# Performance work log

Measured on AMD Instinct MI355X. Metric: run time of the kernel, lower is better.

Reference implementation:

```python
import jax, jax.numpy as jnp
import numpy as np

TOP_K = 2
BALANCE_W = 0.01


def setup_inputs() -> dict:
    key = jax.random.key(0)
    ks = jax.random.split(key, 9)
    B, T, D, E, H, S = 4, 2048, 1024, 16, 1024, 2

    def w(k, shape):
        return jax.random.normal(k, shape, jnp.float32) * 0.02

    return {
        "x": jax.random.normal(ks[0], (B, T, D), jnp.float32),
        "router_w": w(ks[1], (D, E)),
        "router_bias": jnp.zeros((E,), jnp.float32),
        "Wg": w(ks[2], (E, D, H)),
        "Wu": w(ks[3], (E, D, H)),
        "Wd": w(ks[4], (E, H, D)),
        "sWg": w(ks[5], (D, S * H)),
        "sWu": w(ks[6], (D, S * H)),
        "sWd": w(ks[7], (S * H, D)),
    }


def reference(x, router_w, router_bias, Wg, Wu, Wd, sWg, sWu, sWd):
    B, T, D = x.shape
    E = router_w.shape[1]
    flat = x.reshape(-1, D)                      # [N, D], N = B*T
    N = flat.shape[0]

    # ---- router (fp32, matching x.float() in torch ref) ----
    logits = flat @ router_w                     # [N, E]
    probs = jax.nn.softmax(logits, axis=-1)      # unbiased probs
    _, indices = jax.lax.top_k(logits + router_bias, TOP_K)  # [N, K]
    weights = jnp.take_along_axis(probs, indices, axis=-1)   # [N, K]
    weights = weights / jnp.maximum(weights.sum(-1, keepdims=True), 1e-9)

    # per-(token, expert) combine weight; top-k indices are unique per row
    C = jnp.zeros((N, E), flat.dtype).at[jnp.arange(N)[:, None], indices].add(weights)
    expert_load = jax.nn.one_hot(indices, E, dtype=jnp.float32).sum((0, 1))  # [E]

    # ---- routed SwiGLU experts: scan over experts, masked combine ----
    def body(acc, per_e):
        wg, wu, wd, c = per_e                    # [D,H],[D,H],[H,D],[N]
        h = jax.nn.silu(flat @ wg) * (flat @ wu) # [N, H]
        return acc + (h @ wd) * c[:, None], None

    routed, _ = jax.lax.scan(body, jnp.zeros_like(flat), (Wg, Wu, Wd, C.T))

    # ---- shared expert ----
    shared = (jax.nn.silu(flat @ sWg) * (flat @ sWu)) @ sWd

    out = (routed + shared).reshape(B, T, D)

    # ---- Switch/DeepSeek balance loss (training mode) ----
    expert_fraction = expert_load / (N * TOP_K)
    probability_fraction = probs.mean(0)
    balance = BALANCE_W * E * jnp.sum(expert_fraction * probability_fraction)

    return out, balance, expert_load
```

## Files before the change

kernel.cpp:

```cpp
#include <hip/hip_runtime.h>
#include <stdint.h>

#define N_TOK 8192
#define DDIM  1024
#define NEXP  16
#define HDIM  1024
#define SHDIM 2048
#define TM 128
#define BK 64
#define MT_R 144

#define SH_GU_NT  (SHDIM / 64)
#define SH_GU_WGS ((N_TOK / TM) * SH_GU_NT)
#define RT_GU_NT  (HDIM / 64)
#define RT_GU_WGS (MT_R * RT_GU_NT)
#define GU_WGS    (SH_GU_WGS + RT_GU_WGS)

#define TND 128
#define DN_NT     (DDIM / TND)
#define SH_DN_WGS ((N_TOK / TM) * DN_NT)
#define RT_DN_WGS (MT_R * DN_NT)
#define DN_WGS    (SH_DN_WGS + RT_DN_WGS)

#define CPAD 16

typedef __bf16 bf16x8 __attribute__((ext_vector_type(8)));
typedef float  f32x4  __attribute__((ext_vector_type(4)));

__device__ __forceinline__ unsigned short f2bf(float f) {
  union { float f; unsigned u; } v; v.f = f;
  unsigned r = v.u + 0x7fffu + ((v.u >> 16) & 1u);
  return (unsigned short)(r >> 16);
}
__device__ __forceinline__ float bf2f(unsigned short u) {
  union { unsigned u; float f; } v; v.u = (unsigned)u << 16; return v.f;
}

__device__ __forceinline__ void gload16(const void* g, void* l) {
  __builtin_amdgcn_global_load_lds(
      (const __attribute__((address_space(1))) void*)g,
      (__attribute__((address_space(3))) void*)l, 16, 0, 0);
}

__device__ __forceinline__ int xcd_swizzle() {
  int nwg = (int)gridDim.x;
  int b = (int)blockIdx.x;
  return (b & 7) * (nwg >> 3) + (b >> 3);
}


__global__ void k_zero(int* cnt, int* cursor, float* probsum) {
  int t = threadIdx.x;
  if (t < NEXP * CPAD) { cnt[t] = 0; cursor[t] = 0; probsum[t] = 0.f; }
}

__global__ __launch_bounds__(256) void k_router(
    const float* __restrict__ x, const float* __restrict__ rw,
    const float* __restrict__ rb, int* __restrict__ cnt,
    int* __restrict__ tok_idx, float* __restrict__ tok_w,
    float* __restrict__ probs, unsigned short* __restrict__ Xbf) {
  __shared__ float rwT[NEXP * 1024];
  const int t = threadIdx.x;
  {
    int dbase = t >> 2, e0 = (t & 3) * 4;
#pragma unroll
    for (int c = 0; c < 16; c++) {
      int d = dbase + 64 * c;
      float4 v = *(const float4*)(rw + (size_t)d * NEXP + e0);
      rwT[(e0 + 0) * 1024 + d] = v.x;
      rwT[(e0 + 1) * 1024 + d] = v.y;
      rwT[(e0 + 2) * 1024 + d] = v.z;
      rwT[(e0 + 3) * 1024 + d] = v.w;
    }
  }
  __syncthreads();
  const int lane = t & 63, wv = t >> 6;
  const int tok0 = blockIdx.x * 16 + wv * 4;
  float acc[4][NEXP];
#pragma unroll
  for (int tt = 0; tt < 4; tt++)
#pragma unroll
    for (int e = 0; e < NEXP; e++) acc[tt][e] = 0.f;

#pragma unroll
  for (int c = 0; c < 4; c++) {
    int d = lane * 4 + 256 * c;
    float4 xv[4];
#pragma unroll
    for (int tt = 0; tt < 4; tt++) {
      xv[tt] = *(const float4*)(x + (size_t)(tok0 + tt) * DDIM + d);
      ushort4 o;
      o.x = f2bf(xv[tt].x); o.y = f2bf(xv[tt].y);
      o.z = f2bf(xv[tt].z); o.w = f2bf(xv[tt].w);
      *(ushort4*)(Xbf + (size_t)(tok0 + tt) * DDIM + d) = o;
    }
#pragma unroll
    for (int e = 0; e < NEXP; e++) {
      float4 w4 = *(const float4*)(&rwT[e * 1024 + d]);
#pragma unroll
      for (int tt = 0; tt < 4; tt++) {
        acc[tt][e] = fmaf(xv[tt].x, w4.x, acc[tt][e]);
        acc[tt][e] = fmaf(xv[tt].y, w4.y, acc[tt][e]);
        acc[tt][e] = fmaf(xv[tt].z, w4.z, acc[tt][e]);
        acc[tt][e] = fmaf(xv[tt].w, w4.w, acc[tt][e]);
      }
    }
  }
#pragma unroll
  for (int tt = 0; tt < 4; tt++)
#pragma unroll
    for (int e = 0; e < NEXP; e++) {
      float v = acc[tt][e];
#pragma unroll
      for (int o = 32; o; o >>= 1) v += __shfl_xor(v, o);
      acc[tt][e] = v;
    }

#pragma unroll
  for (int tt = 0; tt < 4; tt++) {
    if (lane == tt) {
      int tok = tok0 + tt;
      float mx = acc[tt][0];
#pragma unroll
      for (int e = 1; e < NEXP; e++) mx = fmaxf(mx, acc[tt][e]);
      float p[NEXP]; float s = 0.f;
#pragma unroll
      for (int e = 0; e < NEXP; e++) { p[e] = __expf(acc[tt][e] - mx); s += p[e]; }
      float inv = 1.f / s;
      float* pdst = probs + (size_t)tok * NEXP;
#pragma unroll
      for (int e = 0; e < NEXP; e++) { p[e] *= inv; pdst[e] = p[e]; }
      int i0 = 0; float b0 = acc[tt][0] + rb[0];
#pragma unroll
      for (int e = 1; e < NEXP; e++) { float v = acc[tt][e] + rb[e]; if (v > b0) { b0 = v; i0 = e; } }
      int i1 = -1; float b1 = -3.4e38f;
#pragma unroll
      for (int e = 0; e < NEXP; e++) {
        if (e == i0) continue;
        float v = acc[tt][e] + rb[e]; if (v > b1) { b1 = v; i1 = e; }
      }
      float w0 = 0.f, w1 = 0.f;
#pragma unroll
      for (int e = 0; e < NEXP; e++) { if (e == i0) w0 = p[e]; if (e == i1) w1 = p[e]; }
      float ssum = fmaxf(w0 + w1, 1e-9f);
      w0 /= ssum; w1 /= ssum;
      atomicAdd(&cnt[i0 * CPAD], 1); atomicAdd(&cnt[i1 * CPAD], 1);
      tok_idx[tok * 2]     = i0; tok_idx[tok * 2 + 1] = i1;
      tok_w[tok * 2]       = w0; tok_w[tok * 2 + 1]   = w1;
    }
  }
}

__global__ __launch_bounds__(256) void k_psum(
    const float* __restrict__ probs, float* __restrict__ probsum) {
  __shared__ float ps[NEXP];
  const int t = threadIdx.x;
  if (t < NEXP) ps[t] = 0.f;
  __syncthreads();
  int e = t & 15, trow = t >> 4;
  float s = 0.f;
#pragma unroll
  for (int c = 0; c < 8; c++) {
    int tok = blockIdx.x * 128 + c * 16 + trow;
    s += probs[(size_t)tok * NEXP + e];
  }
  atomicAdd(&ps[e], s);
  __syncthreads();
  if (t < NEXP) atomicAdd(&probsum[t * CPAD], ps[t]);
}

__global__ void k_prefix(const int* __restrict__ cnt, int* __restrict__ offs) {
  if (threadIdx.x == 0) {
    int o = 0;
    for (int e = 0; e < NEXP; e++) { offs[e] = o; o += ((cnt[e * CPAD] + 127) & ~127); }
    offs[NEXP] = o;
  }
}

__global__ __launch_bounds__(256) void k_assign(
    const int* __restrict__ tok_idx, const float* __restrict__ tok_w,
    int* __restrict__ cursor, const int* __restrict__ offs,
    int* __restrict__ row_token, int* __restrict__ tok_rows) {
  int i = blockIdx.x * 256 + threadIdx.x;
  if (i >= N_TOK * 2) return;
  int e = tok_idx[i];
  int pos = atomicAdd(&cursor[e * CPAD], 1);
  int row = offs[e] + pos;
  row_token[row] = i >> 1;
  tok_rows[i] = row;
}


__device__ __forceinline__ void do_transpose64(
    const float* __restrict__ src, unsigned short* __restrict__ dst,
    int R, int C, int tc, int tr, float* tile ) {
  int rx = threadIdx.x >> 4;
  int cx = (threadIdx.x & 15) * 4;
#pragma unroll
  for (int p = 0; p < 4; p++) {
    int r = p * 16 + rx;
    float4 v = *(const float4*)(src + (size_t)(tr + r) * C + tc + cx);
    tile[(cx + 0) * 65 + r] = v.x;
    tile[(cx + 1) * 65 + r] = v.y;
    tile[(cx + 2) * 65 + r] = v.z;
    tile[(cx + 3) * 65 + r] = v.w;
  }
  __syncthreads();
#pragma unroll
  for (int p = 0; p < 4; p++) {
    int c = p * 16 + rx;
    float v0 = tile[c * 65 + cx + 0];
    float v1 = tile[c * 65 + cx + 1];
    float v2 = tile[c * 65 + cx + 2];
    float v3 = tile[c * 65 + cx + 3];
    ushort4 o; o.x = f2bf(v0); o.y = f2bf(v1); o.z = f2bf(v2); o.w = f2bf(v3);
    *(ushort4*)(dst + (size_t)(tc + c) * R + tr + cx) = o;
  }
}

__global__ __launch_bounds__(256) void k_transpose_big(
    const float* __restrict__ Wg, const float* __restrict__ Wu,
    const float* __restrict__ Wd, unsigned short* __restrict__ WgT,
    unsigned short* __restrict__ WuT, unsigned short* __restrict__ WdT) {
  __shared__ float tile[64 * 65];
  int id = blockIdx.x;
  int which = id >> 12;
  int rem = id & 4095;
  int mat = rem >> 8;
  int tl  = rem & 255;
  int bx = tl & 15, by = tl >> 4;
  const float* src = (which == 0 ? Wg : which == 1 ? Wu : Wd) + (size_t)mat * 1024 * 1024;
  unsigned short* dst = (which == 0 ? WgT : which == 1 ? WuT : WdT) + (size_t)mat * 1024 * 1024;
  do_transpose64(src, dst, 1024, 1024, bx * 64, by * 64, tile);
}

__global__ __launch_bounds__(256) void k_transpose_sh(
    const float* __restrict__ sWg, const float* __restrict__ sWu,
    const float* __restrict__ sWd, unsigned short* __restrict__ sWgT,
    unsigned short* __restrict__ sWuT, unsigned short* __restrict__ sWdT) {
  __shared__ float tile[64 * 65];
  int id = blockIdx.x;
  if (id < 1024) {
    const float* src = id < 512 ? sWg : sWu;
    unsigned short* dst = id < 512 ? sWgT : sWuT;
    int tl = id & 511;
    int bx = tl & 31, by = tl >> 5;
    do_transpose64(src, dst, 1024, 2048, bx * 64, by * 64, tile);
  } else {
    int tl = id - 1024;
    int bx = tl & 15, by = tl >> 4;
    do_transpose64(sWd, sWdT, 2048, 1024, bx * 64, by * 64, tile);
  }
}


__global__ __launch_bounds__(256, 4) void k_gateup_all(
    const unsigned short* __restrict__ Xbf,
    const unsigned short* __restrict__ sWgT,
    const unsigned short* __restrict__ sWuT,
    const unsigned short* __restrict__ WgT,
    const unsigned short* __restrict__ WuT,
    unsigned short* __restrict__ Hs,
    unsigned short* __restrict__ Hr,
    const int* __restrict__ offs, const int* __restrict__ cnt,
    const int* __restrict__ row_token) {
  __shared__ unsigned short As[TM * BK];
  __shared__ unsigned short Bgs[64 * BK];
  __shared__ unsigned short Bus[64 * BK];

  const int wg = xcd_swizzle();
  const int t = threadIdx.x;
  const int lane = t & 63, wv = t >> 6;
  const int lr  = lane >> 3;
  const int kbx = (lane & 7) ^ lr;

  int tm, tn, validEnd, Nh;
  const unsigned short *Bgp, *Bup;
  unsigned short* Hout;
  const unsigned short* pA[4];

  if (wg < SH_GU_WGS) {
    int band = wg >> 9;
    int r = wg & 511;
    tm = (r >> 3) * TM;
    tn = (band * 8 + (r & 7)) * 64;
    validEnd = 0x7fffffff;
    Bgp = sWgT; Bup = sWuT;
    Hout = Hs; Nh = SHDIM;
#pragma unroll
    for (int j = 0; j < 4; j++)
      pA[j] = Xbf + (size_t)(tm + (wv * 4 + j) * 8 + lr) * DDIM;
  } else {
    int u = wg - SH_GU_WGS;
    int band = u / 1152;
    int r = u % 1152;
    tm = (r >> 3) * TM;
    tn = (band * 8 + (r & 7)) * 64;
    if (tm >= offs[NEXP]) return;
    int e = 0;
#pragma unroll
    for (int i = 1; i < NEXP; i++) if (tm >= offs[i]) e = i;
    validEnd = offs[e] + cnt[e * CPAD];
    Bgp = WgT + (size_t)e * HDIM * DDIM;
    Bup = WuT + (size_t)e * HDIM * DDIM;
    Hout = Hr; Nh = HDIM;
#pragma unroll
    for (int j = 0; j < 4; j++) {
      int row = tm + (wv * 4 + j) * 8 + lr;
      int tok = row < validEnd ? row_token[row] : 0;
      pA[j] = Xbf + (size_t)tok * DDIM;
    }
  }
  const unsigned short* pBg[2];
  const unsigned short* pBu[2];
#pragma unroll
  for (int j = 0; j < 2; j++) {
    int row = tn + (wv * 2 + j) * 8 + lr;
    pBg[j] = Bgp + (size_t)row * DDIM;
    pBu[j] = Bup + (size_t)row * DDIM;
  }

  auto stage = [&](int k0) {
#pragma unroll
    for (int j = 0; j < 4; j++)
      gload16(pA[j] + k0 + kbx * 8, (void*)&As[(wv * 4 + j) * 512]);
#pragma unroll
    for (int j = 0; j < 2; j++) {
      gload16(pBg[j] + k0 + kbx * 8, (void*)&Bgs[(wv * 2 + j) * 512]);
      gload16(pBu[j] + k0 + kbx * 8, (void*)&Bus[(wv * 2 + j) * 512]);
    }
  };

  f32x4 accG[4][2] = {};
  f32x4 accU[4][2] = {};
  const int wr = wv >> 1, wc = wv & 1;
  const int rbase = lane & 15;
  const int kgrp = lane >> 4;

  for (int k0 = 0; k0 < DDIM; k0 += BK) {
    if (k0) __syncthreads();
    stage(k0);
    __syncthreads();
#pragma unroll
    for (int kk = 0; kk < 2; kk++) {
      bf16x8 af[4], gf[2], uf[2];
      int kbl = kk * 4 + kgrp;
#pragma unroll
      for (int i = 0; i < 4; i++) {
        int r = wr * 64 + i * 16 + rbase;
        af[i] = *(const bf16x8*)((const char*)&As[0] + r * 128 + ((kbl ^ (r & 7)) << 4));
      }
#pragma unroll
      for (int j = 0; j < 2; j++) {
        int r = wc * 32 + j * 16 + rbase;
        gf[j] = *(const bf16x8*)((const char*)&Bgs[0] + r * 128 + ((kbl ^ (r & 7)) << 4));
        uf[j] = *(const bf16x8*)((const char*)&Bus[0] + r * 128 + ((kbl ^ (r & 7)) << 4));
      }
#pragma unroll
      for (int i = 0; i < 4; i++)
#pragma unroll
        for (int j = 0; j < 2; j++) {
          accG[i][j] = __builtin_amdgcn_mfma_f32_16x16x32_bf16(af[i], gf[j], accG[i][j], 0, 0, 0);
          accU[i][j] = __builtin_amdgcn_mfma_f32_16x16x32_bf16(af[i], uf[j], accU[i][j], 0, 0, 0);
        }
    }
  }

  const int orow0 = tm + wr * 64 + (lane >> 4) * 4;
  const int ocol0 = tn + wc * 32 + (lane & 15);
#pragma unroll
  for (int i = 0; i < 4; i++)
#pragma unroll
    for (int j = 0; j < 2; j++)
#pragma unroll
      for (int r = 0; r < 4; r++) {
        int row = orow0 + i * 16 + r;
        if (row < validEnd) {
          float g = accG[i][j][r], u = accU[i][j][r];
          float h = g / (1.f + __expf(-g)) * u;
          Hout[(size_t)row * Nh + ocol0 + j * 16] = f2bf(h);
        }
      }
}

__global__ __launch_bounds__(256, 4) void k_down_all(
    const unsigned short* __restrict__ Hs,
    const unsigned short* __restrict__ Hr,
    const unsigned short* __restrict__ sWdT,
    const unsigned short* __restrict__ WdT,
    float* __restrict__ out,
    unsigned short* __restrict__ Rbuf,
    const int* __restrict__ offs, const int* __restrict__ cnt) {
  __shared__ unsigned short As[TM * BK];
  __shared__ unsigned short Bs[TND * BK];

  const int wg = xcd_swizzle();
  const int t = threadIdx.x;
  const int lane = t & 63, wv = t >> 6;
  const int lr  = lane >> 3;
  const int kbx = (lane & 7) ^ lr;

  int tm, tn, validEnd, K;
  bool routed;
  const unsigned short* pA[4];
  const unsigned short* pB[4];

  if (wg < SH_DN_WGS) {
    routed = false; K = SHDIM;
    tm = (wg >> 3) * TM;
    tn = (wg & 7) * TND;
    validEnd = 0x7fffffff;
#pragma unroll
    for (int j = 0; j < 4; j++) {
      pA[j] = Hs + (size_t)(tm + (wv * 4 + j) * 8 + lr) * SHDIM;
      pB[j] = sWdT + (size_t)(tn + (wv * 4 + j) * 8 + lr) * SHDIM;
    }
  } else {
    routed = true; K = HDIM;
    int wgr = wg - SH_DN_WGS;
    tm = (wgr >> 3) * TM;
    tn = (wgr & 7) * TND;
    if (tm >= offs[NEXP]) return;
    int e = 0;
#pragma unroll
    for (int i = 1; i < NEXP; i++) if (tm >= offs[i]) e = i;
    validEnd = offs[e] + cnt[e * CPAD];
    const unsigned short* B = WdT + (size_t)e * DDIM * HDIM;
#pragma unroll
    for (int j = 0; j < 4; j++) {
      pA[j] = Hr + (size_t)(tm + (wv * 4 + j) * 8 + lr) * HDIM;
      pB[j] = B + (size_t)(tn + (wv * 4 + j) * 8 + lr) * HDIM;
    }
  }

  auto stage = [&](int k0) {
#pragma unroll
    for (int j = 0; j < 4; j++) {
      gload16(pA[j] + k0 + kbx * 8, (void*)&As[(wv * 4 + j) * 512]);
      gload16(pB[j] + k0 + kbx * 8, (void*)&Bs[(wv * 4 + j) * 512]);
    }
  };

  f32x4 acc[4][4] = {};
  const int wr = wv >> 1, wc = wv & 1;
  const int rbase = lane & 15;
  const int kgrp = lane >> 4;

  for (int k0 = 0; k0 < K; k0 += BK) {
    if (k0) __syncthreads();
    stage(k0);
    __syncthreads();
#pragma unroll
    for (int kk = 0; kk < 2; kk++) {
      bf16x8 af[4], bf[4];
      int kbl = kk * 4 + kgrp;
#pragma unroll
      for (int i = 0; i < 4; i++) {
        int r = wr * 64 + i * 16 + rbase;
        af[i] = *(const bf16x8*)((const char*)&As[0] + r * 128 + ((kbl ^ (r & 7)) << 4));
      }
#pragma unroll
      for (int j = 0; j < 4; j++) {
        int r = wc * 64 + j * 16 + rbase;
        bf[j] = *(const bf16x8*)((const char*)&Bs[0] + r * 128 + ((kbl ^ (r & 7)) << 4));
      }
#pragma unroll
      for (int i = 0; i < 4; i++)
#pragma unroll
        for (int j = 0; j < 4; j++)
          acc[i][j] = __builtin_amdgcn_mfma_f32_16x16x32_bf16(af[i], bf[j], acc[i][j], 0, 0, 0);
    }
  }

  const int orow0 = tm + wr * 64 + (lane >> 4) * 4;
  const int ocol0 = tn + wc * 64 + (lane & 15);
#pragma unroll
  for (int i = 0; i < 4; i++)
#pragma unroll
    for (int j = 0; j < 4; j++)
#pragma unroll
      for (int r = 0; r < 4; r++) {
        int row = orow0 + i * 16 + r;
        int col = ocol0 + j * 16;
        if (routed) {
          if (row < validEnd) Rbuf[(size_t)row * DDIM + col] = f2bf(acc[i][j][r]);
        } else {
          out[(size_t)row * DDIM + col] = acc[i][j][r];
        }
      }
}

__global__ __launch_bounds__(256) void k_combine(
    float* __restrict__ out, const unsigned short* __restrict__ Rbuf,
    const int* __restrict__ tok_rows, const float* __restrict__ tok_w) {
  int tok = blockIdx.x;
  int c = threadIdx.x;
  int r0 = tok_rows[tok * 2], r1 = tok_rows[tok * 2 + 1];
  float w0 = tok_w[tok * 2],  w1 = tok_w[tok * 2 + 1];
  float4 o  = ((const float4*)(out + (size_t)tok * DDIM))[c];
  ushort4 a = ((const ushort4*)(Rbuf + (size_t)r0 * DDIM))[c];
  ushort4 b = ((const ushort4*)(Rbuf + (size_t)r1 * DDIM))[c];
  o.x += w0 * bf2f(a.x) + w1 * bf2f(b.x);
  o.y += w0 * bf2f(a.y) + w1 * bf2f(b.y);
  o.z += w0 * bf2f(a.z) + w1 * bf2f(b.z);
  o.w += w0 * bf2f(a.w) + w1 * bf2f(b.w);
  ((float4*)(out + (size_t)tok * DDIM))[c] = o;
}

__global__ void k_tail(const float* __restrict__ probsum, const int* __restrict__ cnt,
                       float* __restrict__ out_tail) {
  if (threadIdx.x == 0) {
    float bal = 0.f;
    for (int e = 0; e < NEXP; e++) {
      float frac = (float)cnt[e * CPAD] / (float)(N_TOK * 2);
      bal += frac * (probsum[e * CPAD] / (float)N_TOK);
    }
    out_tail[0] = 0.01f * (float)NEXP * bal;
  }
  if (threadIdx.x < NEXP) out_tail[1 + threadIdx.x] = (float)cnt[threadIdx.x * CPAD];
}


extern "C" void kernel_launch(void* const* d_in, const int* in_sizes, int n_in,
                              void* d_out, int out_size, void* d_ws, size_t ws_size,
                              hipStream_t stream) {
  const float* x   = (const float*)d_in[0];
  const float* rw  = (const float*)d_in[1];
  const float* rb  = (const float*)d_in[2];
  const float* Wg  = (const float*)d_in[3];
  const float* Wu  = (const float*)d_in[4];
  const float* Wd  = (const float*)d_in[5];
  const float* sWg = (const float*)d_in[6];
  const float* sWu = (const float*)d_in[7];
  const float* sWd = (const float*)d_in[8];
  float* out = (float*)d_out;

  uint8_t* w = (uint8_t*)d_ws;
  size_t off = 0;
  auto alloc = [&](size_t bytes) -> void* {
    void* p = w + off;
    off += (bytes + 255) & ~(size_t)255;
    return p;
  };

  int*   cnt      = (int*)alloc(NEXP * CPAD * 4);
  int*   cursor   = (int*)alloc(NEXP * CPAD * 4);
  float* probsum  = (float*)alloc(NEXP * CPAD * 4);
  int*   offs     = (int*)alloc((NEXP + 1) * 4);
  int*   tok_idx  = (int*)alloc((size_t)N_TOK * 2 * 4);
  float* tok_w    = (float*)alloc((size_t)N_TOK * 2 * 4);
  int*   tok_rows = (int*)alloc((size_t)N_TOK * 2 * 4);
  int*   row_tok  = (int*)alloc((size_t)MT_R * TM * 4);
  float* probs    = (float*)alloc((size_t)N_TOK * NEXP * 4);
  unsigned short* Xbf  = (unsigned short*)alloc((size_t)N_TOK * DDIM * 2);
  unsigned short* Hs   = (unsigned short*)alloc((size_t)N_TOK * SHDIM * 2);
  unsigned short* Hr   = (unsigned short*)alloc((size_t)MT_R * TM * HDIM * 2);
  unsigned short* Rbuf = (unsigned short*)alloc((size_t)MT_R * TM * DDIM * 2);
  unsigned short* WgT  = (unsigned short*)alloc((size_t)NEXP * HDIM * DDIM * 2);
  unsigned short* WuT  = (unsigned short*)alloc((size_t)NEXP * HDIM * DDIM * 2);
  unsigned short* WdT  = (unsigned short*)alloc((size_t)NEXP * DDIM * HDIM * 2);
  unsigned short* sWgT = (unsigned short*)alloc((size_t)SHDIM * DDIM * 2);
  unsigned short* sWuT = (unsigned short*)alloc((size_t)SHDIM * DDIM * 2);
  unsigned short* sWdT = (unsigned short*)alloc((size_t)DDIM * SHDIM * 2);

  if (off > ws_size) return;

  k_zero<<<1, 256, 0, stream>>>(cnt, cursor, probsum);
  k_router<<<N_TOK / 16, 256, 0, stream>>>(x, rw, rb, cnt, tok_idx, tok_w, probs, Xbf);
  k_psum<<<64, 256, 0, stream>>>(probs, probsum);
  k_prefix<<<1, 1, 0, stream>>>(cnt, offs);
  k_assign<<<(N_TOK * 2) / 256, 256, 0, stream>>>(tok_idx, tok_w, cursor, offs, row_tok, tok_rows);

  k_transpose_big<<<12288, 256, 0, stream>>>(Wg, Wu, Wd, WgT, WuT, WdT);
  k_transpose_sh<<<1536, 256, 0, stream>>>(sWg, sWu, sWd, sWgT, sWuT, sWdT);

  k_gateup_all<<<GU_WGS, 256, 0, stream>>>(
      Xbf, sWgT, sWuT, WgT, WuT, Hs, Hr, offs, cnt, row_tok);
  k_down_all<<<DN_WGS, 256, 0, stream>>>(
      Hs, Hr, sWdT, WdT, out, Rbuf, offs, cnt);
  k_combine<<<N_TOK, 256, 0, stream>>>(out, Rbuf, tok_rows, tok_w);

  k_tail<<<1, 32, 0, stream>>>(probsum, cnt, out + (size_t)N_TOK * DDIM);
}
```

Before: 426.5 us.

## Fuse router bookkeeping kernels and overlap down-weight transposes with gate-up GEMM

Folds the probability-sum reduction into the router via shared-memory atomics, which removes the probs buffer and the k_psum launch. Prefix offsets are now recomputed per block from the counts, which removes k_prefix. The assign step is merged into the gate/up weight transpose kernel, and the down-projection weight transposes run as extra workgroups inside the gate-up GEMM launch so they overlap with its compute. The balance-loss tail moves into the combine kernel and the occupancy hint is raised to 5. In exchange it adds per-block redundant offset computation and couples transpose work with GEMM scheduling.

```diff
diff --git a/kernel.cpp b/kernel.cpp
--- a/kernel.cpp
+++ b/kernel.cpp
@@ -10,17 +10,22 @@
 #define BK 64
 #define MT_R 144
 
-#define SH_GU_NT  (SHDIM / 64)
-#define SH_GU_WGS ((N_TOK / TM) * SH_GU_NT)
-#define RT_GU_NT  (HDIM / 64)
-#define RT_GU_WGS (MT_R * RT_GU_NT)
-#define GU_WGS    (SH_GU_WGS + RT_GU_WGS)
+#define SH_GU_NT  32
+#define SH_GU_WGS 2048
+#define RT_GU_NT  16
+#define RT_GU_WGS 2304
+#define GU_WGS    4352
+#define GU_SLOTS  (GU_WGS / 8)
+#define TR2_WGS   4608
+#define TR2_SLOTS (TR2_WGS / 8)
+#define GUF_WGS   (GU_WGS + TR2_WGS)
 
 #define TND 128
-#define DN_NT     (DDIM / TND)
-#define SH_DN_WGS ((N_TOK / TM) * DN_NT)
-#define RT_DN_WGS (MT_R * DN_NT)
-#define DN_WGS    (SH_DN_WGS + RT_DN_WGS)
+#define DN_WGS    1664
+
+#define TR1_WGS   9216
+#define ASG_WGS   64
+#define T1A_WGS   (TR1_WGS + ASG_WGS)
 
 #define CPAD 16
 
@@ -48,6 +53,13 @@
   return (b & 7) * (nwg >> 3) + (b >> 3);
 }
 
+__device__ __forceinline__ void calc_offs(const int* __restrict__ cnt, int* offs) {
+  int o = 0;
+#pragma unroll
+  for (int e = 0; e < NEXP; e++) { offs[e] = o; o += ((cnt[e * CPAD] + 127) & ~127); }
+  offs[NEXP] = o;
+}
+
 
 __global__ void k_zero(int* cnt, int* cursor, float* probsum) {
   int t = threadIdx.x;
@@ -58,9 +70,11 @@
     const float* __restrict__ x, const float* __restrict__ rw,
     const float* __restrict__ rb, int* __restrict__ cnt,
     int* __restrict__ tok_idx, float* __restrict__ tok_w,
-    float* __restrict__ probs, unsigned short* __restrict__ Xbf) {
+    float* __restrict__ probsum, unsigned short* __restrict__ Xbf) {
   __shared__ float rwT[NEXP * 1024];
+  __shared__ float ps[NEXP];
   const int t = threadIdx.x;
+  if (t < NEXP) ps[t] = 0.f;
   {
     int dbase = t >> 2, e0 = (t & 3) * 4;
 #pragma unroll
@@ -127,9 +141,8 @@
 #pragma unroll
       for (int e = 0; e < NEXP; e++) { p[e] = __expf(acc[tt][e] - mx); s += p[e]; }
       float inv = 1.f / s;
-      float* pdst = probs + (size_t)tok * NEXP;
-#pragma unroll
-      for (int e = 0; e < NEXP; e++) { p[e] *= inv; pdst[e] = p[e]; }
+#pragma unroll
+      for (int e = 0; e < NEXP; e++) { p[e] *= inv; atomicAdd(&ps[e], p[e]); }
       int i0 = 0; float b0 = acc[tt][0] + rb[0];
 #pragma unroll
       for (int e = 1; e < NEXP; e++) { float v = acc[tt][e] + rb[e]; if (v > b0) { b0 = v; i0 = e; } }
@@ -149,45 +162,8 @@
       tok_w[tok * 2]       = w0; tok_w[tok * 2 + 1]   = w1;
     }
   }
-}
-
-__global__ __launch_bounds__(256) void k_psum(
-    const float* __restrict__ probs, float* __restrict__ probsum) {
-  __shared__ float ps[NEXP];
-  const int t = threadIdx.x;
-  if (t < NEXP) ps[t] = 0.f;
-  __syncthreads();
-  int e = t & 15, trow = t >> 4;
-  float s = 0.f;
-#pragma unroll
-  for (int c = 0; c < 8; c++) {
-    int tok = blockIdx.x * 128 + c * 16 + trow;
-    s += probs[(size_t)tok * NEXP + e];
-  }
-  atomicAdd(&ps[e], s);
   __syncthreads();
   if (t < NEXP) atomicAdd(&probsum[t * CPAD], ps[t]);
-}
-
-__global__ void k_prefix(const int* __restrict__ cnt, int* __restrict__ offs) {
-  if (threadIdx.x == 0) {
-    int o = 0;
-    for (int e = 0; e < NEXP; e++) { offs[e] = o; o += ((cnt[e * CPAD] + 127) & ~127); }
-    offs[NEXP] = o;
-  }
-}
-
-__global__ __launch_bounds__(256) void k_assign(
-    const int* __restrict__ tok_idx, const float* __restrict__ tok_w,
-    int* __restrict__ cursor, const int* __restrict__ offs,
-    int* __restrict__ row_token, int* __restrict__ tok_rows) {
-  int i = blockIdx.x * 256 + threadIdx.x;
-  if (i >= N_TOK * 2) return;
-  int e = tok_idx[i];
-  int pos = atomicAdd(&cursor[e * CPAD], 1);
-  int row = offs[e] + pos;
-  row_token[row] = i >> 1;
-  tok_rows[i] = row;
 }
 
 
@@ -218,43 +194,44 @@
   }
 }
 
-__global__ __launch_bounds__(256) void k_transpose_big(
+__global__ __launch_bounds__(256) void k_trgu_assign(
     const float* __restrict__ Wg, const float* __restrict__ Wu,
-    const float* __restrict__ Wd, unsigned short* __restrict__ WgT,
-    unsigned short* __restrict__ WuT, unsigned short* __restrict__ WdT) {
+    const float* __restrict__ sWg, const float* __restrict__ sWu,
+    unsigned short* __restrict__ WgT, unsigned short* __restrict__ WuT,
+    unsigned short* __restrict__ sWgT, unsigned short* __restrict__ sWuT,
+    const int* __restrict__ tok_idx, int* __restrict__ cursor,
+    const int* __restrict__ cnt, int* __restrict__ row_token,
+    int* __restrict__ tok_rows) {
   __shared__ float tile[64 * 65];
   int id = blockIdx.x;
-  int which = id >> 12;
-  int rem = id & 4095;
-  int mat = rem >> 8;
-  int tl  = rem & 255;
-  int bx = tl & 15, by = tl >> 4;
-  const float* src = (which == 0 ? Wg : which == 1 ? Wu : Wd) + (size_t)mat * 1024 * 1024;
-  unsigned short* dst = (which == 0 ? WgT : which == 1 ? WuT : WdT) + (size_t)mat * 1024 * 1024;
-  do_transpose64(src, dst, 1024, 1024, bx * 64, by * 64, tile);
-}
-
-__global__ __launch_bounds__(256) void k_transpose_sh(
-    const float* __restrict__ sWg, const float* __restrict__ sWu,
-    const float* __restrict__ sWd, unsigned short* __restrict__ sWgT,
-    unsigned short* __restrict__ sWuT, unsigned short* __restrict__ sWdT) {
-  __shared__ float tile[64 * 65];
-  int id = blockIdx.x;
-  if (id < 1024) {
-    const float* src = id < 512 ? sWg : sWu;
-    unsigned short* dst = id < 512 ? sWgT : sWuT;
-    int tl = id & 511;
-    int bx = tl & 31, by = tl >> 5;
-    do_transpose64(src, dst, 1024, 2048, bx * 64, by * 64, tile);
+  if (id < 4096) {
+    int mat = id >> 8, tl = id & 255;
+    do_transpose64(Wg + ((size_t)mat << 20), WgT + ((size_t)mat << 20),
+                   1024, 1024, (tl & 15) * 64, (tl >> 4) * 64, tile);
+  } else if (id < 8192) {
+    int mat = (id - 4096) >> 8, tl = id & 255;
+    do_transpose64(Wu + ((size_t)mat << 20), WuT + ((size_t)mat << 20),
+                   1024, 1024, (tl & 15) * 64, (tl >> 4) * 64, tile);
+  } else if (id < 8704) {
+    int tl = id - 8192;
+    do_transpose64(sWg, sWgT, 1024, 2048, (tl & 31) * 64, (tl >> 5) * 64, tile);
+  } else if (id < TR1_WGS) {
+    int tl = id - 8704;
+    do_transpose64(sWu, sWuT, 1024, 2048, (tl & 31) * 64, (tl >> 5) * 64, tile);
   } else {
-    int tl = id - 1024;
-    int bx = tl & 15, by = tl >> 4;
-    do_transpose64(sWd, sWdT, 2048, 1024, bx * 64, by * 64, tile);
-  }
-}
-
-
-__global__ __launch_bounds__(256, 4) void k_gateup_all(
+    int i = (id - TR1_WGS) * 256 + threadIdx.x;
+    int offs[NEXP + 1];
+    calc_offs(cnt, offs);
+    int e = tok_idx[i];
+    int pos = atomicAdd(&cursor[e * CPAD], 1);
+    int row = offs[e] + pos;
+    row_token[row] = i >> 1;
+    tok_rows[i] = row;
+  }
+}
+
+
+__global__ __launch_bounds__(256, 5) void k_gateup_all(
     const unsigned short* __restrict__ Xbf,
     const unsigned short* __restrict__ sWgT,
     const unsigned short* __restrict__ sWuT,
@@ -262,13 +239,33 @@
     const unsigned short* __restrict__ WuT,
     unsigned short* __restrict__ Hs,
     unsigned short* __restrict__ Hr,
-    const int* __restrict__ offs, const int* __restrict__ cnt,
-    const int* __restrict__ row_token) {
-  __shared__ unsigned short As[TM * BK];
-  __shared__ unsigned short Bgs[64 * BK];
-  __shared__ unsigned short Bus[64 * BK];
-
-  const int wg = xcd_swizzle();
+    const int* __restrict__ cnt,
+    const int* __restrict__ row_token,
+    const float* __restrict__ Wd, const float* __restrict__ sWd,
+    unsigned short* __restrict__ WdT, unsigned short* __restrict__ sWdT) {
+  __shared__ __attribute__((aligned(16))) char smem[32768];
+  unsigned short* As  = (unsigned short*)smem;
+  unsigned short* Bgs = (unsigned short*)(smem + 16384);
+  unsigned short* Bus = (unsigned short*)(smem + 24576);
+
+  const int slot = blockIdx.x >> 3;
+  const int xcd  = blockIdx.x & 7;
+
+  if (slot >= GU_SLOTS) {
+    int tid = xcd * TR2_SLOTS + (slot - GU_SLOTS);
+    float* tile = (float*)smem;
+    if (tid < 4096) {
+      int mat = tid >> 8, tl = tid & 255;
+      do_transpose64(Wd + ((size_t)mat << 20), WdT + ((size_t)mat << 20),
+                     1024, 1024, (tl & 15) * 64, (tl >> 4) * 64, tile);
+    } else {
+      int tl = tid - 4096;
+      do_transpose64(sWd, sWdT, 2048, 1024, (tl & 15) * 64, (tl >> 4) * 64, tile);
+    }
+    return;
+  }
+
+  const int wg = xcd * GU_SLOTS + slot;
   const int t = threadIdx.x;
   const int lane = t & 63, wv = t >> 6;
   const int lr  = lane >> 3;
@@ -296,6 +293,8 @@
     int r = u % 1152;
     tm = (r >> 3) * TM;
     tn = (band * 8 + (r & 7)) * 64;
+    int offs[NEXP + 1];
+    calc_offs(cnt, offs);
     if (tm >= offs[NEXP]) return;
     int e = 0;
 #pragma unroll
@@ -348,13 +347,13 @@
 #pragma unroll
       for (int i = 0; i < 4; i++) {
         int r = wr * 64 + i * 16 + rbase;
-        af[i] = *(const bf16x8*)((const char*)&As[0] + r * 128 + ((kbl ^ (r & 7)) << 4));
+        af[i] = *(const bf16x8*)((const char*)As + r * 128 + ((kbl ^ (r & 7)) << 4));
       }
 #pragma unroll
       for (int j = 0; j < 2; j++) {
         int r = wc * 32 + j * 16 + rbase;
-        gf[j] = *(const bf16x8*)((const char*)&Bgs[0] + r * 128 + ((kbl ^ (r & 7)) << 4));
-        uf[j] = *(const bf16x8*)((const char*)&Bus[0] + r * 128 + ((kbl ^ (r & 7)) << 4));
+        gf[j] = *(const bf16x8*)((const char*)Bgs + r * 128 + ((kbl ^ (r & 7)) << 4));
+        uf[j] = *(const bf16x8*)((const char*)Bus + r * 128 + ((kbl ^ (r & 7)) << 4));
       }
 #pragma unroll
       for (int i = 0; i < 4; i++)
@@ -383,14 +382,14 @@
       }
 }
 
-__global__ __launch_bounds__(256, 4) void k_down_all(
+__global__ __launch_bounds__(256, 5) void k_down_all(
     const unsigned short* __restrict__ Hs,
     const unsigned short* __restrict__ Hr,
     const unsigned short* __restrict__ sWdT,
     const unsigned short* __restrict__ WdT,
     float* __restrict__ out,
     unsigned short* __restrict__ Rbuf,
-    const int* __restrict__ offs, const int* __restrict__ cnt) {
+    const int* __restrict__ cnt) {
   __shared__ unsigned short As[TM * BK];
   __shared__ unsigned short Bs[TND * BK];
 
@@ -405,7 +404,7 @@
   const unsigned short* pA[4];
   const unsigned short* pB[4];
 
-  if (wg < SH_DN_WGS) {
+  if (wg < 512) {
     routed = false; K = SHDIM;
     tm = (wg >> 3) * TM;
     tn = (wg & 7) * TND;
@@ -417,9 +416,11 @@
     }
   } else {
     routed = true; K = HDIM;
-    int wgr = wg - SH_DN_WGS;
+    int wgr = wg - 512;
     tm = (wgr >> 3) * TM;
     tn = (wgr & 7) * TND;
+    int offs[NEXP + 1];
+    calc_offs(cnt, offs);
     if (tm >= offs[NEXP]) return;
     int e = 0;
 #pragma unroll
@@ -492,7 +493,9 @@
 
 __global__ __launch_bounds__(256) void k_combine(
     float* __restrict__ out, const unsigned short* __restrict__ Rbuf,
-    const int* __restrict__ tok_rows, const float* __restrict__ tok_w) {
+    const int* __restrict__ tok_rows, const float* __restrict__ tok_w,
+    const float* __restrict__ probsum, const int* __restrict__ cnt,
+    float* __restrict__ out_tail) {
   int tok = blockIdx.x;
   int c = threadIdx.x;
   int r0 = tok_rows[tok * 2], r1 = tok_rows[tok * 2 + 1];
@@ -505,19 +508,18 @@
   o.z += w0 * bf2f(a.z) + w1 * bf2f(b.z);
   o.w += w0 * bf2f(a.w) + w1 * bf2f(b.w);
   ((float4*)(out + (size_t)tok * DDIM))[c] = o;
-}
-
-__global__ void k_tail(const float* __restrict__ probsum, const int* __restrict__ cnt,
-                       float* __restrict__ out_tail) {
-  if (threadIdx.x == 0) {
-    float bal = 0.f;
-    for (int e = 0; e < NEXP; e++) {
-      float frac = (float)cnt[e * CPAD] / (float)(N_TOK * 2);
-      bal += frac * (probsum[e * CPAD] / (float)N_TOK);
-    }
-    out_tail[0] = 0.01f * (float)NEXP * bal;
-  }
-  if (threadIdx.x < NEXP) out_tail[1 + threadIdx.x] = (float)cnt[threadIdx.x * CPAD];
+
+  if (blockIdx.x == 0) {
+    if (threadIdx.x == 0) {
+      float bal = 0.f;
+      for (int e = 0; e < NEXP; e++) {
+        float frac = (float)cnt[e * CPAD] / (float)(N_TOK * 2);
+        bal += frac * (probsum[e * CPAD] / (float)N_TOK);
+      }
+      out_tail[0] = 0.01f * (float)NEXP * bal;
+    }
+    if (threadIdx.x < NEXP) out_tail[1 + threadIdx.x] = (float)cnt[threadIdx.x * CPAD];
+  }
 }
 
 
@@ -546,12 +548,10 @@
   int*   cnt      = (int*)alloc(NEXP * CPAD * 4);
   int*   cursor   = (int*)alloc(NEXP * CPAD * 4);
   float* probsum  = (float*)alloc(NEXP * CPAD * 4);
-  int*   offs     = (int*)alloc((NEXP + 1) * 4);
   int*   tok_idx  = (int*)alloc((size_t)N_TOK * 2 * 4);
   float* tok_w    = (float*)alloc((size_t)N_TOK * 2 * 4);
   int*   tok_rows = (int*)alloc((size_t)N_TOK * 2 * 4);
   int*   row_tok  = (int*)alloc((size_t)MT_R * TM * 4);
-  float* probs    = (float*)alloc((size_t)N_TOK * NEXP * 4);
   unsigned short* Xbf  = (unsigned short*)alloc((size_t)N_TOK * DDIM * 2);
   unsigned short* Hs   = (unsigned short*)alloc((size_t)N_TOK * SHDIM * 2);
   unsigned short* Hr   = (unsigned short*)alloc((size_t)MT_R * TM * HDIM * 2);
@@ -566,19 +566,15 @@
   if (off > ws_size) return;
 
   k_zero<<<1, 256, 0, stream>>>(cnt, cursor, probsum);
-  k_router<<<N_TOK / 16, 256, 0, stream>>>(x, rw, rb, cnt, tok_idx, tok_w, probs, Xbf);
-  k_psum<<<64, 256, 0, stream>>>(probs, probsum);
-  k_prefix<<<1, 1, 0, stream>>>(cnt, offs);
-  k_assign<<<(N_TOK * 2) / 256, 256, 0, stream>>>(tok_idx, tok_w, cursor, offs, row_tok, tok_rows);
-
-  k_transpose_big<<<12288, 256, 0, stream>>>(Wg, Wu, Wd, WgT, WuT, WdT);
-  k_transpose_sh<<<1536, 256, 0, stream>>>(sWg, sWu, sWd, sWgT, sWuT, sWdT);
-
-  k_gateup_all<<<GU_WGS, 256, 0, stream>>>(
-      Xbf, sWgT, sWuT, WgT, WuT, Hs, Hr, offs, cnt, row_tok);
+  k_router<<<N_TOK / 16, 256, 0, stream>>>(x, rw, rb, cnt, tok_idx, tok_w, probsum, Xbf);
+  k_trgu_assign<<<T1A_WGS, 256, 0, stream>>>(
+      Wg, Wu, sWg, sWu, WgT, WuT, sWgT, sWuT,
+      tok_idx, cursor, cnt, row_tok, tok_rows);
+  k_gateup_all<<<GUF_WGS, 256, 0, stream>>>(
+      Xbf, sWgT, sWuT, WgT, WuT, Hs, Hr, cnt, row_tok,
+      Wd, sWd, WdT, sWdT);
   k_down_all<<<DN_WGS, 256, 0, stream>>>(
-      Hs, Hr, sWdT, WdT, out, Rbuf, offs, cnt);
-  k_combine<<<N_TOK, 256, 0, stream>>>(out, Rbuf, tok_rows, tok_w);
-
-  k_tail<<<1, 32, 0, stream>>>(probsum, cnt, out + (size_t)N_TOK * DDIM);
-}
+      Hs, Hr, sWdT, WdT, out, Rbuf, cnt);
+  k_combine<<<N_TOK, 256, 0, stream>>>(
+      out, Rbuf, tok_rows, tok_w, probsum, cnt, out + (size_t)N_TOK * DDIM);
+}
```

Measured after the change: 1.022 ms. 2.4x slower.
